# Kernel tuning notes

Measured on AMD Instinct MI355X. Metric: run time of the kernel, lower is better.

## Reference

```python
import jax, jax.numpy as jnp
import numpy as np

NUM_HEADS = 8
LN_EPS = 1e-5


def layer_norm(x, g, b):
    mu = jnp.mean(x, axis=-1, keepdims=True)
    var = jnp.mean(jnp.square(x - mu), axis=-1, keepdims=True)
    return (x - mu) / jnp.sqrt(var + LN_EPS) * g + b


def setup_inputs() -> dict:
    key = jax.random.key(0)
    ks = jax.random.split(key, 16)
    B, N, D, F = 16, 1024, 256, 1024
    s = 0.02
    return {
        "x": jax.random.normal(ks[0], (B, N, D), jnp.float32),
        "spatial_encoding": jax.random.normal(ks[1], (B, N, N), jnp.float32),
        "edge_encoding": jax.random.normal(ks[2], (B, N, N), jnp.float32),
        "gamma1": jnp.ones((D,), jnp.float32),
        "beta1": jnp.zeros((D,), jnp.float32),
        "gamma2": jnp.ones((D,), jnp.float32),
        "beta2": jnp.zeros((D,), jnp.float32),
        "Wq": jax.random.normal(ks[3], (D, D), jnp.float32) * s,
        "Wk": jax.random.normal(ks[4], (D, D), jnp.float32) * s,
        "Wv": jax.random.normal(ks[5], (D, D), jnp.float32) * s,
        "Wo": jax.random.normal(ks[6], (D, D), jnp.float32) * s,
        "W1": jax.random.normal(ks[7], (F, D), jnp.float32) * s,
        "b1": jnp.zeros((F,), jnp.float32),
        "W2": jax.random.normal(ks[8], (D, F), jnp.float32) * s,
        "b2": jnp.zeros((D,), jnp.float32),
    }


def reference(x, spatial_encoding, edge_encoding, gamma1, beta1, gamma2, beta2,
              Wq, Wk, Wv, Wo, W1, b1, W2, b2):
    B, N, D = x.shape
    H = NUM_HEADS
    hd = D // H
    scale = D ** (-0.5)  # source scales by hidden_dim, not head_size

    att_in = layer_norm(x, gamma1, beta1)

    def proj(W):  # [B,N,D] -> [B,H,N,hd]
        return (att_in @ W.T).reshape(B, N, H, hd).transpose(0, 2, 1, 3)

    q, k, v = proj(Wq), proj(Wk), proj(Wv)
    bias = (spatial_encoding + edge_encoding)[:, None]  # [B,1,N,N]
    a = jnp.einsum('bhnd,bhmd->bhnm', q, k) * scale + bias
    pad_mask = jnp.any(a != 0, axis=-1)  # [B,H,N]
    a = jnp.where(pad_mask[..., None], a, -jnp.inf)
    p = jnp.nan_to_num(jax.nn.softmax(a, axis=-1))
    o = jnp.einsum('bhnm,bhmd->bhnd', p, v)
    attn = o.transpose(0, 2, 1, 3).reshape(B, N, D) @ Wo.T
    att_output = attn + x

    pad_mask2 = jnp.any(att_output == 0, axis=-1)  # [B,N]
    ffn_in = layer_norm(x, gamma2, beta2)  # note: norm of x per the source
    h = jax.nn.gelu(ffn_in @ W1.T + b1, approximate=True)
    ffn_out = h @ W2.T + b2 + att_output
    return jnp.where(pad_mask2[..., None], 0.0, ffn_out)
```

## Files before the change

kernel.cpp:

```cpp
#include <hip/hip_runtime.h>
#include <hip/hip_bf16.h>
#include <math.h>

#define Bq 16
#define Nq 1024
#define Dq 256
#define Fq 1024
#define Hq 8
#define HDq 32
#define Mq (Bq * Nq)
#define SCALE 0.0625f
#define LN_EPS 1e-5f

typedef __attribute__((ext_vector_type(8))) short short8;
typedef __attribute__((ext_vector_type(4))) float f32x4;

__device__ __forceinline__ float bf2f(unsigned short s) {
    unsigned u = ((unsigned)s) << 16;
    return __builtin_bit_cast(float, u);
}
__device__ __forceinline__ unsigned short f2bf(float f) {
    __hip_bfloat16 h = __float2bfloat16(f);
    return __builtin_bit_cast(unsigned short, h);
}

typedef __attribute__((address_space(3))) unsigned int lds_uint;
typedef const __attribute__((address_space(1))) unsigned int glb_uint;
__device__ __forceinline__ void async16(void* lds, const void* g) {
    __builtin_amdgcn_global_load_lds((glb_uint*)g, (lds_uint*)lds, 16, 0, 0);
}

__device__ __forceinline__ float gelu_tanh(float v) {
    const float c = 0.7978845608028654f;
    float u = c * (v + 0.044715f * v * v * v);
    return 0.5f * v * (1.0f + tanhf(u));
}

__global__ __launch_bounds__(256) void cvt_weights(
    const float* __restrict__ Wq, const float* __restrict__ Wk,
    const float* __restrict__ Wv, const float* __restrict__ Wo,
    const float* __restrict__ W1, const float* __restrict__ W2,
    unsigned short* __restrict__ dst)
{
    const int blk = blockIdx.x;
    int seg, local;
    if (blk < 256)      { seg = blk >> 6; local = blk & 63; }
    else if (blk < 512) { seg = 4; local = blk - 256; }
    else                { seg = 5; local = blk - 512; }
    const float* srcs[6] = {Wq, Wk, Wv, Wo, W1, W2};
    const size_t dsto[6] = {0, 65536, 131072, 196608, 262144, 524288};
    const float* src = srcs[seg] + (size_t)local * 1024;
    unsigned short* d = dst + dsto[seg] + (size_t)local * 1024;
    const int t4 = threadIdx.x * 4;
    float4 v = *(const float4*)(src + t4);
    uint2 o;
    o.x = (unsigned)f2bf(v.x) | ((unsigned)f2bf(v.y) << 16);
    o.y = (unsigned)f2bf(v.z) | ((unsigned)f2bf(v.w) << 16);
    *(uint2*)(d + t4) = o;
}

__global__ __launch_bounds__(256) void bias_cvt_perm(
    const float* __restrict__ sp, const float* __restrict__ ed,
    unsigned short* __restrict__ P)
{
    const int nt = blockIdx.x, b = blockIdx.y;
    const int t = threadIdx.x;
    __shared__ unsigned short lds[16][1032];
    const size_t src0 = ((size_t)b * Nq + nt * 16) * Nq;

    for (int idx = t; idx < 4096; idx += 256) {
        const int r = idx >> 8, c4 = (idx & 255) * 4;
        float4 a = *(const float4*)(sp + src0 + (size_t)r * Nq + c4);
        float4 e = *(const float4*)(ed + src0 + (size_t)r * Nq + c4);
        uint2 o;
        o.x = (unsigned)f2bf(a.x + e.x) | ((unsigned)f2bf(a.y + e.y) << 16);
        o.y = (unsigned)f2bf(a.z + e.z) | ((unsigned)f2bf(a.w + e.w) << 16);
        *(uint2*)&lds[r][c4] = o;
    }
    __syncthreads();

    unsigned short* Ps = P + ((size_t)(b * 64 + nt) << 14);
    #pragma unroll
    for (int it = 0; it < 8; it++) {
        const int o   = (it * 256 + t) * 8;
        const int r0  = o & 15;
        const int col = (o >> 4) & 15;
        const int m   = (o >> 8) & 7;
        const int tt  = (o >> 11) & 7;
        const int c   = tt * 128 + m * 16 + col;
        uint4 w;
        w.x = (unsigned)lds[r0 + 0][c] | ((unsigned)lds[r0 + 1][c] << 16);
        w.y = (unsigned)lds[r0 + 2][c] | ((unsigned)lds[r0 + 3][c] << 16);
        w.z = (unsigned)lds[r0 + 4][c] | ((unsigned)lds[r0 + 5][c] << 16);
        w.w = (unsigned)lds[r0 + 6][c] | ((unsigned)lds[r0 + 7][c] << 16);
        *(uint4*)(Ps + o) = w;
    }
}

__global__ __launch_bounds__(256) void ln2_kernel(
    const float* __restrict__ x,
    const float* __restrict__ g1, const float* __restrict__ bb1,
    const float* __restrict__ g2, const float* __restrict__ bb2,
    unsigned short* __restrict__ att_in, unsigned short* __restrict__ ffn_in)
{
    const int row = blockIdx.x;
    const int t = threadIdx.x;
    const size_t base = (size_t)row * Dq;
    float v = x[base + t];

    float s = v, sq = v * v;
    #pragma unroll
    for (int off = 32; off > 0; off >>= 1) {
        s  += __shfl_down(s, off);
        sq += __shfl_down(sq, off);
    }
    __shared__ float ssum[4], ssq[4];
    __shared__ float mu_s, rstd_s;
    const int lane = t & 63, wid = t >> 6;
    if (lane == 0) { ssum[wid] = s; ssq[wid] = sq; }
    __syncthreads();
    if (t == 0) {
        float S = ssum[0] + ssum[1] + ssum[2] + ssum[3];
        float Q = ssq[0] + ssq[1] + ssq[2] + ssq[3];
        float mu = S * (1.0f / Dq);
        float var = Q * (1.0f / Dq) - mu * mu;
        mu_s = mu;
        rstd_s = rsqrtf(var + LN_EPS);
    }
    __syncthreads();
    const float nx = (v - mu_s) * rstd_s;
    att_in[base + t] = f2bf(nx * g1[t] + bb1[t]);
    ffn_in[base + t] = f2bf(nx * g2[t] + bb2[t]);
}

#define TM 128
#define TN 128
#define TK 32

__global__ __launch_bounds__(256) void gemm_mfma(
    const unsigned short* __restrict__ A, const unsigned short* __restrict__ W,
    const float* __restrict__ bias, const float* __restrict__ add,
    float* __restrict__ outF, unsigned short* __restrict__ outBF,
    unsigned short* __restrict__ Qb, unsigned short* __restrict__ Kb,
    unsigned short* __restrict__ Vt,
    int M, int Nc, int K, int mode, int apply_gelu)
{
    __shared__ unsigned short As[TM * TK];
    __shared__ unsigned short Bs[TN * TK];
    const int t = threadIdx.x;
    const int w = t >> 6, lane = t & 63;
    const int col = lane & 15, quad = lane >> 4;
    const int wr = w >> 1, wc = w & 1;
    const int row0 = blockIdx.y * TM;
    const int col0 = blockIdx.x * TN;

    f32x4 acc[4][4] = {};

    for (int k0 = 0; k0 < K; k0 += TK) {
        #pragma unroll
        for (int j = 0; j < 2; j++) {
            const int c = w * 128 + j * 64 + lane;
            const int r = c >> 2, seg = c & 3;
            async16(&As[(size_t)(w * 128 + j * 64) * 8],
                    A + (size_t)(row0 + r) * K + k0 + seg * 8);
            async16(&Bs[(size_t)(w * 128 + j * 64) * 8],
                    W + (size_t)(col0 + r) * K + k0 + seg * 8);
        }
        __syncthreads();
        short8 wf[4], af[4];
        #pragma unroll
        for (int i = 0; i < 4; i++)
            wf[i] = *(const short8*)&Bs[(wc * 64 + i * 16 + col) * TK + quad * 8];
        #pragma unroll
        for (int j = 0; j < 4; j++)
            af[j] = *(const short8*)&As[(wr * 64 + j * 16 + col) * TK + quad * 8];
        #pragma unroll
        for (int i = 0; i < 4; i++)
            #pragma unroll
            for (int j = 0; j < 4; j++)
                acc[i][j] = __builtin_amdgcn_mfma_f32_16x16x32_bf16(wf[i], af[j], acc[i][j], 0, 0, 0);
        __syncthreads();
    }

    #pragma unroll
    for (int i = 0; i < 4; i++) {
        #pragma unroll
        for (int j = 0; j < 4; j++) {
            const int c0 = col0 + wc * 64 + i * 16 + quad * 4;
            const int r  = row0 + wr * 64 + j * 16 + col;
            float4 v = make_float4(acc[i][j][0], acc[i][j][1], acc[i][j][2], acc[i][j][3]);
            if (mode == 2 && c0 < 256) { v.x *= SCALE; v.y *= SCALE; v.z *= SCALE; v.w *= SCALE; }
            if (bias) {
                float4 bb = *(const float4*)&bias[c0];
                v.x += bb.x; v.y += bb.y; v.z += bb.z; v.w += bb.w;
            }
            if (apply_gelu) {
                v.x = gelu_tanh(v.x); v.y = gelu_tanh(v.y);
                v.z = gelu_tanh(v.z); v.w = gelu_tanh(v.w);
            }
            if (add) {
                float4 aa = *(const float4*)&add[(size_t)r * Nc + c0];
                v.x += aa.x; v.y += aa.y; v.z += aa.z; v.w += aa.w;
            }
            if (mode == 0) {
                *(float4*)&outF[(size_t)r * Nc + c0] = v;
            } else if (mode == 1) {
                uint2 o;
                o.x = (unsigned)f2bf(v.x) | ((unsigned)f2bf(v.y) << 16);
                o.y = (unsigned)f2bf(v.z) | ((unsigned)f2bf(v.w) << 16);
                *(uint2*)&outBF[(size_t)r * Nc + c0] = o;
            } else {
                const int b = r >> 10, n = r & 1023;
                if (c0 < 512) {
                    const int cq = c0 & 255;
                    const int h = cq >> 5, d0 = cq & 31;
                    unsigned short* dst = (c0 < 256 ? Qb : Kb);
                    uint2 o;
                    o.x = (unsigned)f2bf(v.x) | ((unsigned)f2bf(v.y) << 16);
                    o.y = (unsigned)f2bf(v.z) | ((unsigned)f2bf(v.w) << 16);
                    *(uint2*)&dst[(((size_t)(b * Hq + h) << 10) + n) * HDq + d0] = o;
                } else {
                    const int cv = c0 - 512;
                    const int h = cv >> 5, d0 = cv & 31;
                    unsigned short* dst = Vt + (((size_t)(b * Hq + h) * HDq + d0) << 10) + n;
                    dst[0]      = f2bf(v.x);
                    dst[1024]   = f2bf(v.y);
                    dst[2048]   = f2bf(v.z);
                    dst[3072]   = f2bf(v.w);
                }
            }
        }
    }
}

__global__ __launch_bounds__(512, 2) void attn_mfma(
    const unsigned short* __restrict__ Qbf, const unsigned short* __restrict__ Kbf,
    const unsigned short* __restrict__ Vt, const unsigned short* __restrict__ biasP,
    unsigned short* __restrict__ O16)
{
    const int flat = blockIdx.x;
    const int id2  = (flat & 7) * 32 + (flat >> 3);
    const int b    = id2 >> 4;
    const int h    = (id2 >> 1) & 7;
    const int nh   = id2 & 1;

    const int t = threadIdx.x;
    const int w = t >> 6;
    const int lane = t & 63;
    const int col = lane & 15;
    const int quad = lane >> 4;

    __shared__ unsigned short Klds[32768];
    __shared__ unsigned short Vlds[32768];
    __shared__ unsigned short S16[8][2048];

    const size_t hb = (size_t)b * Hq + h;
    const unsigned short* Qh = Qbf + hb * (Nq * HDq);
    const unsigned short* Kh = Kbf + hb * (Nq * HDq);
    const unsigned short* Vh = Vt  + hb * (HDq * Nq);

    #pragma unroll
    for (int i = 0; i < 8; i++) {
        const int ck = i * 512 + t;
        async16(&Klds[ck * 8], Kh + ((ck * 8) ^ (((ck >> 3) & 3) << 3)));
        async16(&Vlds[ck * 8], Vh + ((ck * 8) ^ (((ck >> 7) & 7) << 3)));
    }

    const int n0 = nh * 512 + w * 64;
    short8 aq[4];
    #pragma unroll
    for (int qt = 0; qt < 4; qt++)
        aq[qt] = *(const short8*)(Qh + (size_t)(n0 + qt * 16 + col) * HDq + quad * 8);

    const unsigned short* Ps0 = biasP + ((size_t)(b * 64 + nh * 32 + w * 4) << 14);
    unsigned short* Sw = &S16[w][0];

    __syncthreads();

    f32x4 o0[4] = {{0.f,0.f,0.f,0.f},{0.f,0.f,0.f,0.f},{0.f,0.f,0.f,0.f},{0.f,0.f,0.f,0.f}};
    f32x4 o1[4] = {{0.f,0.f,0.f,0.f},{0.f,0.f,0.f,0.f},{0.f,0.f,0.f,0.f},{0.f,0.f,0.f,0.f}};
    float rsum[4][4] = {};

    for (int tt = 0; tt < 8; tt++) {
        const int k0 = tt * 128;
        short8 kf[8], vf0[4], vf1[4];
        #pragma unroll
        for (int m = 0; m < 8; m++)
            kf[m] = *(const short8*)&Klds[((k0 + m * 16 + col) * 32 + quad * 8)
                                          ^ (((col >> 1) & 3) << 3)];
        #pragma unroll
        for (int c = 0; c < 4; c++) {
            vf0[c] = *(const short8*)&Vlds[((col << 10) + k0 + c * 32 + quad * 8)
                                           ^ ((col & 7) << 3)];
            vf1[c] = *(const short8*)&Vlds[(((col + 16) << 10) + k0 + c * 32 + quad * 8)
                                           ^ ((col & 7) << 3)];
        }
        #pragma unroll
        for (int qt = 0; qt < 4; qt++) {
            const unsigned short* Psq = Ps0 + (qt << 14) + (tt << 11);
            #pragma unroll
            for (int m = 0; m < 8; m++) {
                f32x4 cc = {0.f, 0.f, 0.f, 0.f};
                cc = __builtin_amdgcn_mfma_f32_16x16x32_bf16(aq[qt], kf[m], cc, 0, 0, 0);
                uint2 bv = *(const uint2*)(Psq + (m << 8) + col * 16 + quad * 4);
                const float bi[4] = {
                    bf2f((unsigned short)(bv.x & 0xffff)), bf2f((unsigned short)(bv.x >> 16)),
                    bf2f((unsigned short)(bv.y & 0xffff)), bf2f((unsigned short)(bv.y >> 16))
                };
                #pragma unroll
                for (int i = 0; i < 4; i++) {
                    const int r = quad * 4 + i;
                    float e = __expf(cc[i] + bi[i]);
                    rsum[qt][i] += e;
                    const int sidx = (r * 128 + m * 16 + col) ^ ((r & 7) << 3);
                    Sw[sidx] = f2bf(e);
                }
            }
            #pragma unroll
            for (int c = 0; c < 4; c++) {
                const int ridx = (col * 128 + c * 32 + quad * 8) ^ ((col & 7) << 3);
                short8 ap = *(const short8*)&Sw[ridx];
                o0[qt] = __builtin_amdgcn_mfma_f32_16x16x32_bf16(ap, vf0[c], o0[qt], 0, 0, 0);
                o1[qt] = __builtin_amdgcn_mfma_f32_16x16x32_bf16(ap, vf1[c], o1[qt], 0, 0, 0);
            }
        }
    }

    #pragma unroll
    for (int qt = 0; qt < 4; qt++) {
        #pragma unroll
        for (int off = 1; off < 16; off <<= 1) {
            #pragma unroll
            for (int i = 0; i < 4; i++) rsum[qt][i] += __shfl_xor(rsum[qt][i], off, 16);
        }
        unsigned short* op = O16 + ((size_t)b * Nq + n0 + qt * 16) * Dq + h * HDq;
        #pragma unroll
        for (int i = 0; i < 4; i++) {
            const float inv = 1.0f / rsum[qt][i];
            const int q = quad * 4 + i;
            op[(size_t)q * Dq + col]      = f2bf(o0[qt][i] * inv);
            op[(size_t)q * Dq + col + 16] = f2bf(o1[qt][i] * inv);
        }
    }
}

__global__ __launch_bounds__(256) void pad2_kernel(
    const float* __restrict__ AO, float* __restrict__ out)
{
    const int row = blockIdx.x;
    const int t = threadIdx.x;
    const float v = AO[(size_t)row * Dq + t];
    unsigned long long m = __ballot(v == 0.0f);
    __shared__ unsigned long long w[4];
    if ((t & 63) == 0) w[t >> 6] = m;
    __syncthreads();
    if ((w[0] | w[1] | w[2] | w[3]) != 0ULL)
        out[(size_t)row * Dq + t] = 0.0f;
}

extern "C" void kernel_launch(void* const* d_in, const int* in_sizes, int n_in,
                              void* d_out, int out_size, void* d_ws, size_t ws_size,
                              hipStream_t stream)
{
    const float* x      = (const float*)d_in[0];
    const float* sp     = (const float*)d_in[1];
    const float* ed     = (const float*)d_in[2];
    const float* gamma1 = (const float*)d_in[3];
    const float* beta1  = (const float*)d_in[4];
    const float* gamma2 = (const float*)d_in[5];
    const float* beta2  = (const float*)d_in[6];
    const float* Wq     = (const float*)d_in[7];
    const float* Wk     = (const float*)d_in[8];
    const float* Wv     = (const float*)d_in[9];
    const float* Wo     = (const float*)d_in[10];
    const float* W1     = (const float*)d_in[11];
    const float* b1     = (const float*)d_in[12];
    const float* W2     = (const float*)d_in[13];
    const float* b2     = (const float*)d_in[14];
    float* out = (float*)d_out;

    unsigned short* s = (unsigned short*)d_ws;
    const size_t MD = (size_t)Mq * Dq;
    unsigned short* att_in16 = s;
    unsigned short* ffn_in16 = s + MD;
    unsigned short* Qbf      = s + 2 * MD;
    unsigned short* Kbf      = s + 3 * MD;
    unsigned short* Vtb      = s + 4 * MD;
    unsigned short* W16      = s + 5 * MD;
    unsigned short* h16      = s + 5 * MD + 786432;
    unsigned short* O16      = att_in16;
    float*          AO       = (float*)Qbf;
    unsigned short* biasP    = h16;

    unsigned short* Wo16 = W16 + 196608;
    unsigned short* W116 = W16 + 262144;
    unsigned short* W216 = W16 + 524288;

    cvt_weights<<<768, 256, 0, stream>>>(Wq, Wk, Wv, Wo, W1, W2, W16);

    bias_cvt_perm<<<dim3(64, 16), 256, 0, stream>>>(sp, ed, biasP);

    ln2_kernel<<<Mq, 256, 0, stream>>>(x, gamma1, beta1, gamma2, beta2, att_in16, ffn_in16);

    dim3 gQKV(768 / TN, Mq / TM);
    gemm_mfma<<<gQKV, 256, 0, stream>>>(att_in16, W16, nullptr, nullptr, nullptr, nullptr,
                                        Qbf, Kbf, Vtb, Mq, 768, Dq, 2, 0);

    attn_mfma<<<256, 512, 0, stream>>>(Qbf, Kbf, Vtb, biasP, O16);

    dim3 gP(Dq / TN, Mq / TM);
    gemm_mfma<<<gP, 256, 0, stream>>>(O16, Wo16, nullptr, x, AO, nullptr,
                                      nullptr, nullptr, nullptr, Mq, Dq, Dq, 0, 0);

    dim3 gF1(Fq / TN, Mq / TM);
    gemm_mfma<<<gF1, 256, 0, stream>>>(ffn_in16, W116, b1, nullptr, nullptr, h16,
                                       nullptr, nullptr, nullptr, Mq, Fq, Dq, 1, 1);

    gemm_mfma<<<gP, 256, 0, stream>>>(h16, W216, b2, AO, out, nullptr,
                                      nullptr, nullptr, nullptr, Mq, Dq, Fq, 0, 0);

    pad2_kernel<<<Mq, 256, 0, stream>>>(AO, out);
}
```

Baseline: 426.6 us.

## Double-buffer GEMM LDS tiles and use 16 waves per attention block

The GEMM kernel gets double-buffered LDS tiles so the async loads for the next K slice are issued while MFMAs run on the current one, with a single barrier per iteration. The attention kernel moves from 8 to 16 waves per block, each handling 32 query rows over 64-key chunks. The bias permutation kernel's layout is changed to match the new 64-column chunking. This aims to hide global-load latency and give each CU more waves. The cost is more LDS per block and higher register pressure under launch_bounds(1024,4), which could cause spills.

```diff
diff --git a/kernel.cpp b/kernel.cpp
--- a/kernel.cpp
+++ b/kernel.cpp
@@ -85,9 +85,8 @@
         const int o   = (it * 256 + t) * 8;
         const int r0  = o & 15;
         const int col = (o >> 4) & 15;
-        const int m   = (o >> 8) & 7;
-        const int tt  = (o >> 11) & 7;
-        const int c   = tt * 128 + m * 16 + col;
+        const int mq  = (o >> 8) & 63;
+        const int c   = mq * 16 + col;
         uint4 w;
         w.x = (unsigned)lds[r0 + 0][c] | ((unsigned)lds[r0 + 1][c] << 16);
         w.y = (unsigned)lds[r0 + 2][c] | ((unsigned)lds[r0 + 3][c] << 16);
@@ -145,8 +144,8 @@
     unsigned short* __restrict__ Vt,
     int M, int Nc, int K, int mode, int apply_gelu)
 {
-    __shared__ unsigned short As[TM * TK];
-    __shared__ unsigned short Bs[TN * TK];
+    __shared__ unsigned short As[2][TM * TK];
+    __shared__ unsigned short Bs[2][TN * TK];
     const int t = threadIdx.x;
     const int w = t >> 6, lane = t & 63;
     const int col = lane & 15, quad = lane >> 4;
@@ -156,31 +155,41 @@
 
     f32x4 acc[4][4] = {};
 
+    const int c0s = w * 128 + lane;
+    const int c1s = c0s + 64;
+    const int r0s = c0s >> 2, s0s = (c0s & 3) * 8;
+    const int r1s = c1s >> 2, s1s = (c1s & 3) * 8;
+
+#define STAGE(buf, kk)                                                        \
+    do {                                                                      \
+        async16(&As[buf][(w * 128) * 8],      A + (size_t)(row0 + r0s) * K + (kk) + s0s); \
+        async16(&Bs[buf][(w * 128) * 8],      W + (size_t)(col0 + r0s) * K + (kk) + s0s); \
+        async16(&As[buf][(w * 128 + 64) * 8], A + (size_t)(row0 + r1s) * K + (kk) + s1s); \
+        async16(&Bs[buf][(w * 128 + 64) * 8], W + (size_t)(col0 + r1s) * K + (kk) + s1s); \
+    } while (0)
+
+    STAGE(0, 0);
+    __syncthreads();
+
+    int cur = 0;
     for (int k0 = 0; k0 < K; k0 += TK) {
-        #pragma unroll
-        for (int j = 0; j < 2; j++) {
-            const int c = w * 128 + j * 64 + lane;
-            const int r = c >> 2, seg = c & 3;
-            async16(&As[(size_t)(w * 128 + j * 64) * 8],
-                    A + (size_t)(row0 + r) * K + k0 + seg * 8);
-            async16(&Bs[(size_t)(w * 128 + j * 64) * 8],
-                    W + (size_t)(col0 + r) * K + k0 + seg * 8);
-        }
-        __syncthreads();
+        if (k0 + TK < K) STAGE(cur ^ 1, k0 + TK);
         short8 wf[4], af[4];
         #pragma unroll
         for (int i = 0; i < 4; i++)
-            wf[i] = *(const short8*)&Bs[(wc * 64 + i * 16 + col) * TK + quad * 8];
+            wf[i] = *(const short8*)&Bs[cur][(wc * 64 + i * 16 + col) * TK + quad * 8];
         #pragma unroll
         for (int j = 0; j < 4; j++)
-            af[j] = *(const short8*)&As[(wr * 64 + j * 16 + col) * TK + quad * 8];
+            af[j] = *(const short8*)&As[cur][(wr * 64 + j * 16 + col) * TK + quad * 8];
         #pragma unroll
         for (int i = 0; i < 4; i++)
             #pragma unroll
             for (int j = 0; j < 4; j++)
                 acc[i][j] = __builtin_amdgcn_mfma_f32_16x16x32_bf16(wf[i], af[j], acc[i][j], 0, 0, 0);
         __syncthreads();
-    }
+        cur ^= 1;
+    }
+#undef STAGE
 
     #pragma unroll
     for (int i = 0; i < 4; i++) {
@@ -233,7 +242,7 @@
     }
 }
 
-__global__ __launch_bounds__(512, 2) void attn_mfma(
+__global__ __launch_bounds__(1024, 4) void attn_mfma(
     const unsigned short* __restrict__ Qbf, const unsigned short* __restrict__ Kbf,
     const unsigned short* __restrict__ Vt, const unsigned short* __restrict__ biasP,
     unsigned short* __restrict__ O16)
@@ -252,7 +261,7 @@
 
     __shared__ unsigned short Klds[32768];
     __shared__ unsigned short Vlds[32768];
-    __shared__ unsigned short S16[8][2048];
+    __shared__ unsigned short S16[16][1024];
 
     const size_t hb = (size_t)b * Hq + h;
     const unsigned short* Qh = Qbf + hb * (Nq * HDq);
@@ -260,46 +269,46 @@
     const unsigned short* Vh = Vt  + hb * (HDq * Nq);
 
     #pragma unroll
-    for (int i = 0; i < 8; i++) {
-        const int ck = i * 512 + t;
+    for (int i = 0; i < 4; i++) {
+        const int ck = i * 1024 + t;
         async16(&Klds[ck * 8], Kh + ((ck * 8) ^ (((ck >> 3) & 3) << 3)));
         async16(&Vlds[ck * 8], Vh + ((ck * 8) ^ (((ck >> 7) & 7) << 3)));
     }
 
-    const int n0 = nh * 512 + w * 64;
-    short8 aq[4];
-    #pragma unroll
-    for (int qt = 0; qt < 4; qt++)
+    const int n0 = nh * 512 + w * 32;
+    short8 aq[2];
+    #pragma unroll
+    for (int qt = 0; qt < 2; qt++)
         aq[qt] = *(const short8*)(Qh + (size_t)(n0 + qt * 16 + col) * HDq + quad * 8);
 
-    const unsigned short* Ps0 = biasP + ((size_t)(b * 64 + nh * 32 + w * 4) << 14);
+    const unsigned short* Ps0 = biasP + ((size_t)(b * 64 + nh * 32 + w * 2) << 14);
     unsigned short* Sw = &S16[w][0];
 
     __syncthreads();
 
-    f32x4 o0[4] = {{0.f,0.f,0.f,0.f},{0.f,0.f,0.f,0.f},{0.f,0.f,0.f,0.f},{0.f,0.f,0.f,0.f}};
-    f32x4 o1[4] = {{0.f,0.f,0.f,0.f},{0.f,0.f,0.f,0.f},{0.f,0.f,0.f,0.f},{0.f,0.f,0.f,0.f}};
-    float rsum[4][4] = {};
-
-    for (int tt = 0; tt < 8; tt++) {
-        const int k0 = tt * 128;
-        short8 kf[8], vf0[4], vf1[4];
-        #pragma unroll
-        for (int m = 0; m < 8; m++)
+    f32x4 o0[2] = {{0.f,0.f,0.f,0.f},{0.f,0.f,0.f,0.f}};
+    f32x4 o1[2] = {{0.f,0.f,0.f,0.f},{0.f,0.f,0.f,0.f}};
+    float rsum[2][4] = {};
+
+    for (int tt = 0; tt < 16; tt++) {
+        const int k0 = tt * 64;
+        short8 kf[4], vf0[2], vf1[2];
+        #pragma unroll
+        for (int m = 0; m < 4; m++)
             kf[m] = *(const short8*)&Klds[((k0 + m * 16 + col) * 32 + quad * 8)
                                           ^ (((col >> 1) & 3) << 3)];
         #pragma unroll
-        for (int c = 0; c < 4; c++) {
+        for (int c = 0; c < 2; c++) {
             vf0[c] = *(const short8*)&Vlds[((col << 10) + k0 + c * 32 + quad * 8)
                                            ^ ((col & 7) << 3)];
             vf1[c] = *(const short8*)&Vlds[(((col + 16) << 10) + k0 + c * 32 + quad * 8)
                                            ^ ((col & 7) << 3)];
         }
         #pragma unroll
-        for (int qt = 0; qt < 4; qt++) {
-            const unsigned short* Psq = Ps0 + (qt << 14) + (tt << 11);
+        for (int qt = 0; qt < 2; qt++) {
+            const unsigned short* Psq = Ps0 + (qt << 14) + (k0 << 4);
             #pragma unroll
-            for (int m = 0; m < 8; m++) {
+            for (int m = 0; m < 4; m++) {
                 f32x4 cc = {0.f, 0.f, 0.f, 0.f};
                 cc = __builtin_amdgcn_mfma_f32_16x16x32_bf16(aq[qt], kf[m], cc, 0, 0, 0);
                 uint2 bv = *(const uint2*)(Psq + (m << 8) + col * 16 + quad * 4);
@@ -312,13 +321,13 @@
                     const int r = quad * 4 + i;
                     float e = __expf(cc[i] + bi[i]);
                     rsum[qt][i] += e;
-                    const int sidx = (r * 128 + m * 16 + col) ^ ((r & 7) << 3);
+                    const int sidx = (r * 64 + m * 16 + col) ^ ((r & 7) << 3);
                     Sw[sidx] = f2bf(e);
                 }
             }
             #pragma unroll
-            for (int c = 0; c < 4; c++) {
-                const int ridx = (col * 128 + c * 32 + quad * 8) ^ ((col & 7) << 3);
+            for (int c = 0; c < 2; c++) {
+                const int ridx = (col * 64 + c * 32 + quad * 8) ^ ((col & 7) << 3);
                 short8 ap = *(const short8*)&Sw[ridx];
                 o0[qt] = __builtin_amdgcn_mfma_f32_16x16x32_bf16(ap, vf0[c], o0[qt], 0, 0, 0);
                 o1[qt] = __builtin_amdgcn_mfma_f32_16x16x32_bf16(ap, vf1[c], o1[qt], 0, 0, 0);
@@ -327,7 +336,7 @@
     }
 
     #pragma unroll
-    for (int qt = 0; qt < 4; qt++) {
+    for (int qt = 0; qt < 2; qt++) {
         #pragma unroll
         for (int off = 1; off < 16; off <<= 1) {
             #pragma unroll
@@ -406,7 +415,7 @@
     gemm_mfma<<<gQKV, 256, 0, stream>>>(att_in16, W16, nullptr, nullptr, nullptr, nullptr,
                                         Qbf, Kbf, Vtb, Mq, 768, Dq, 2, 0);
 
-    attn_mfma<<<256, 512, 0, stream>>>(Qbf, Kbf, Vtb, biasP, O16);
+    attn_mfma<<<256, 1024, 0, stream>>>(Qbf, Kbf, Vtb, biasP, O16);
 
     dim3 gP(Dq / TN, Mq / TM);
     gemm_mfma<<<gP, 256, 0, stream>>>(O16, Wo16, nullptr, x, AO, nullptr,
```

Measured after the change: 385.8 us. 1.11x faster.
